# Kernel tuning notes

Hardware: AMD Instinct MI355X
Metric: run time of the kernel (lower is better)

The kernel has to match this reference:

```python
import jax, jax.numpy as jnp
import numpy as np
import math

HEAD_DIM = 256
NUM_HEADS = 8
NUM_KV_HEADS = 1
ROPE_THETA = 10000.0


def _rope_cos_sin(position_ids, dim, base, dtype):
    # inv_freq: [dim//2]
    inv_freq = 1.0 / (base ** (jnp.arange(0, dim, 2, dtype=jnp.float32) / dim))
    # freqs: [B, S, dim//2]
    freqs = position_ids.astype(jnp.float32)[..., None] * inv_freq[None, None, :]
    emb = jnp.concatenate([freqs, freqs], axis=-1)  # [B, S, dim]
    return jnp.cos(emb).astype(dtype), jnp.sin(emb).astype(dtype)


def _rotate_half(x):
    half = x.shape[-1] // 2
    return jnp.concatenate([-x[..., half:], x[..., :half]], axis=-1)


def setup_inputs() -> dict:
    key = jax.random.key(0)
    ks = jax.random.split(key, 6)
    B, S, H = 2, 2048, 2048
    hidden_states = jax.random.normal(ks[0], (B, S, H), dtype=jnp.float32)
    attention_mask = jnp.zeros((B, 1, S, S), dtype=jnp.float32)
    position_ids = jnp.arange(B * S, dtype=jnp.int64).reshape(B, S) % S
    wq = jax.random.normal(ks[1], (H, NUM_HEADS * HEAD_DIM), dtype=jnp.float32) * 0.02
    wk = jax.random.normal(ks[2], (H, NUM_KV_HEADS * HEAD_DIM), dtype=jnp.float32) * 0.02
    wv = jax.random.normal(ks[3], (H, NUM_KV_HEADS * HEAD_DIM), dtype=jnp.float32) * 0.02
    wo = jax.random.normal(ks[4], (NUM_HEADS * HEAD_DIM, H), dtype=jnp.float32) * 0.02
    return {"hidden_states": hidden_states, "attention_mask": attention_mask,
            "position_ids": position_ids, "wq": wq, "wk": wk, "wv": wv, "wo": wo}


def reference(hidden_states, attention_mask, position_ids, wq, wk, wv, wo):
    B, S, _ = hidden_states.shape
    q = (hidden_states @ wq).reshape(B, S, NUM_HEADS, HEAD_DIM).transpose(0, 2, 1, 3)
    k = (hidden_states @ wk).reshape(B, S, NUM_KV_HEADS, HEAD_DIM).transpose(0, 2, 1, 3)
    v = (hidden_states @ wv).reshape(B, S, NUM_KV_HEADS, HEAD_DIM).transpose(0, 2, 1, 3)

    cos, sin = _rope_cos_sin(position_ids, HEAD_DIM, ROPE_THETA, hidden_states.dtype)
    cos = cos[:, None, :, :]  # [B,1,S,D]
    sin = sin[:, None, :, :]
    q = q * cos + _rotate_half(q) * sin
    k = k * cos + _rotate_half(k) * sin

    # repeat_kv (GQA/MQA expansion)
    n_rep = NUM_HEADS // NUM_KV_HEADS
    k = jnp.repeat(k, n_rep, axis=1)  # [B,H,S,D]
    v = jnp.repeat(v, n_rep, axis=1)

    scores = jnp.einsum('bhqd,bhkd->bhqk', q, k) / math.sqrt(HEAD_DIM)
    scores = scores + attention_mask
    probs = jax.nn.softmax(scores.astype(jnp.float32), axis=-1).astype(q.dtype)
    attn = jnp.einsum('bhqk,bhkd->bhqd', probs, v)  # [B,H,S,D]
    attn = attn.transpose(0, 2, 1, 3).reshape(B, S, NUM_HEADS * HEAD_DIM)
    return attn @ wo
```

## Files before the change

### kernel.cpp

```cpp
#include <hip/hip_runtime.h>
#include <hip/hip_bf16.h>

typedef unsigned short u16;
using f32x4  = __attribute__((ext_vector_type(4))) float;
using bf16x8 = __attribute__((ext_vector_type(8))) __bf16;
using u16x8  = __attribute__((ext_vector_type(8))) unsigned short;
using u16x4  = __attribute__((ext_vector_type(4))) unsigned short;

__device__ __forceinline__ float bf2f(u16 v) {
  union { unsigned u; float f; } x; x.u = ((unsigned)v) << 16; return x.f;
}
__device__ __forceinline__ u16 f2bf(float f) {
  union { float f; unsigned u; } x; x.f = f;
  unsigned r = x.u + 0x7fffu + ((x.u >> 16) & 1u);
  return (u16)(r >> 16);
}
__device__ __forceinline__ void async_load16(const u16* g, u16* l) {
  __builtin_amdgcn_global_load_lds(
      (const __attribute__((address_space(1))) unsigned int*)g,
      (__attribute__((address_space(3))) unsigned int*)l, 16, 0, 0);
}
__device__ __forceinline__ float fexp2(float x) {
#if __has_builtin(__builtin_amdgcn_exp2f)
  return __builtin_amdgcn_exp2f(x);
#else
  return exp2f(x);
#endif
}
__device__ __forceinline__ float vmax4(f32x4 v) {
  return fmaxf(fmaxf(v[0], v[1]), fmaxf(v[2], v[3]));
}
__device__ __forceinline__ int swz_col(int col, int rowk) {
  return (col & ~63) | ((((col >> 3) & 7) ^ rowk) << 3) | (col & 7);
}

__global__ __launch_bounds__(256) void cast_f32_bf16_sw(const float* __restrict__ in,
                                                        u16* __restrict__ out) {
  long i = ((long)blockIdx.x * 256 + threadIdx.x) * 8;
  int m = (int)(i >> 11);
  int col = (int)(i & 2047);
  float4 a = *(const float4*)(in + i);
  float4 b = *(const float4*)(in + i + 4);
  u16x8 v;
  v[0] = f2bf(a.x); v[1] = f2bf(a.y); v[2] = f2bf(a.z); v[3] = f2bf(a.w);
  v[4] = f2bf(b.x); v[5] = f2bf(b.y); v[6] = f2bf(b.z); v[7] = f2bf(b.w);
  *(u16x8*)(out + ((long)m << 11) + swz_col(col, m & 7)) = v;
}

__global__ __launch_bounds__(256) void trans_all(const float* __restrict__ wq,
                                                 const float* __restrict__ wk,
                                                 const float* __restrict__ wv,
                                                 const float* __restrict__ wo,
                                                 u16* __restrict__ wqkvT, u16* __restrict__ woT) {
  const int z = blockIdx.z, bx = blockIdx.x, by = blockIdx.y;
  if (z == 1 && bx >= 64) return;
  const float* src; int srs; u16* dst;
  const int R0 = bx * 32;
  if (z == 0) {
    if (R0 < 2048)      { src = wq + R0;          srs = 2048; }
    else if (R0 < 2304) { src = wk + (R0 - 2048); srs = 256;  }
    else                { src = wv + (R0 - 2304); srs = 256;  }
    dst = wqkvT;
  } else { src = wo + R0; srs = 2048; dst = woT; }
  __shared__ float t[32][33];
  int tx = threadIdx.x, ty = threadIdx.y;
  int br = by * 32;
#pragma unroll
  for (int i = 0; i < 32; i += 8)
    t[ty + i][tx] = src[(long)(br + ty + i) * srs + tx];
  __syncthreads();
#pragma unroll
  for (int i = 0; i < 32; i += 8) {
    int R = R0 + ty + i, C = br + tx;
    dst[(long)R * 2048 + swz_col(C, R & 7)] = f2bf(t[tx][ty + i]);
  }
}

template <typename CT>
__global__ __launch_bounds__(256) void gemm_bt(const u16* __restrict__ A, const u16* __restrict__ Bt,
                                               CT* __restrict__ C, int M, int N, int K) {
  __shared__ __attribute__((aligned(16))) u16 sA[128 * 64];
  __shared__ __attribute__((aligned(16))) u16 sB[128 * 64];
  const int n0 = blockIdx.x * 128, m0 = blockIdx.y * 128;
  const int tid = threadIdx.x;
  const int w = tid >> 6, lane = tid & 63;
  const int l15 = lane & 15, quad = lane >> 4;
  const int wm = (w >> 1) * 64, wn = (w & 1) * 64;
  const int lrow = lane >> 3, lcol = (lane & 7) * 8;
  const u16* Ag = A + (long)(m0 + lrow) * K + lcol;
  const u16* Bg = Bt + (long)(n0 + lrow) * K + lcol;
  const int g0 = ((quad ^ (l15 & 7)) << 3);
  f32x4 acc[4][4] = {};
  for (int k0 = 0; k0 < K; k0 += 64) {
#pragma unroll
    for (int i = 0; i < 4; ++i) {
      int rr = (w * 4 + i) * 8;
      async_load16(Ag + (long)rr * K + k0, &sA[rr * 64]);
      async_load16(Bg + (long)rr * K + k0, &sB[rr * 64]);
    }
    __syncthreads();
#pragma unroll
    for (int kk2 = 0; kk2 < 2; ++kk2) {
      const int go = kk2 ? (g0 ^ 32) : g0;
      bf16x8 af[4], bf[4];
#pragma unroll
      for (int t = 0; t < 4; ++t) {
        af[t] = *(const bf16x8*)&sA[(wm + t * 16 + l15) * 64 + go];
        bf[t] = *(const bf16x8*)&sB[(wn + t * 16 + l15) * 64 + go];
      }
#pragma unroll
      for (int mt = 0; mt < 4; ++mt)
#pragma unroll
        for (int nt = 0; nt < 4; ++nt)
          acc[mt][nt] = __builtin_amdgcn_mfma_f32_16x16x32_bf16(af[mt], bf[nt], acc[mt][nt], 0, 0, 0);
    }
    __syncthreads();
  }
#pragma unroll
  for (int mt = 0; mt < 4; ++mt)
#pragma unroll
    for (int nt = 0; nt < 4; ++nt)
#pragma unroll
      for (int r = 0; r < 4; ++r) {
        long idx = (long)(m0 + wm + mt * 16 + quad * 4 + r) * N + (n0 + wn + nt * 16 + l15);
        if constexpr (sizeof(CT) == 4) C[idx] = acc[mt][nt][r];
        else                           C[idx] = f2bf(acc[mt][nt][r]);
      }
}

__global__ __launch_bounds__(256) void rope_pack(u16* __restrict__ qkv, u16* __restrict__ kp) {
  const int row = blockIdx.x;
  const int tid = threadIdx.x;
  const int d = tid & 127;
  const int s = row & 2047;
  float ang = (float)s * fexp2(-(float)d * 0.10381025296523007f);
  float sn, cs;
  sincosf(ang, &sn, &cs);
  long base = (long)row * 2560;
#pragma unroll
  for (int j = 0; j < 4; ++j) {
    int h = (tid >> 7) + j * 2;
    long p = base + h * 256 + d;
    float x0 = bf2f(qkv[p]), x1 = bf2f(qkv[p + 128]);
    qkv[p]       = f2bf(x0 * cs - x1 * sn);
    qkv[p + 128] = f2bf(x1 * cs + x0 * sn);
  }
  if (tid < 128) {
    long p = base + 2048 + d;
    float x0 = bf2f(qkv[p]), x1 = bf2f(qkv[p + 128]);
    float y0 = x0 * cs - x1 * sn, y1 = x1 * cs + x0 * sn;
    int b = row >> 11, t = (row >> 6) & 31, r = row & 63;
    long sw = (r >> 1) & 7;
    long tb = (long)(b * 32 + t) * 8 * 2048;
#pragma unroll
    for (int u = 0; u < 2; ++u) {
      int D = d + u * 128;
      long off = tb + (long)(D >> 5) * 2048 + r * 32 + (D & 31);
      long off2 = (((off >> 3) ^ sw) << 3) | (off & 7);
      kp[off2] = f2bf(u ? y1 : y0);
    }
  }
}

__global__ __launch_bounds__(256) void pack_vt(const u16* __restrict__ qkv, u16* __restrict__ vp) {
  __shared__ u16 sm[32][40];
  int x = blockIdx.x, y = blockIdx.y, b = blockIdx.z;
  int tx = threadIdx.x, ty = threadIdx.y;
  long inrow = (long)b * 2048 + (y >> 1) * 64 + (y & 1) * 32;
#pragma unroll
  for (int i = 0; i < 32; i += 8)
    sm[ty + i][tx] = qkv[(inrow + ty + i) * 2560 + 2304 + x * 32 + tx];
  __syncthreads();
  long obase = ((long)(b * 32 + (y >> 1)) * 2 + (y & 1)) * 8192 + (long)x * 1024;
#pragma unroll
  for (int i = 0; i < 32; i += 8) {
    long el = obase + (ty + i) * 32 + tx;
    el ^= (long)((((ty + i) >> 1) & 7) << 3);
    vp[el] = sm[tx][ty + i];
  }
}

__global__ __launch_bounds__(512) void flash_attn(const u16* __restrict__ qkv,
                                                  const u16* __restrict__ kp,
                                                  const u16* __restrict__ vp,
                                                  u16* __restrict__ attn) {
  const int qt = blockIdx.x, h = blockIdx.y, b = blockIdx.z;
  const int tid = threadIdx.x, w = tid >> 6, lane = tid & 63;
  const int l15 = lane & 15, quad = lane >> 4;
  __shared__ __attribute__((aligned(16))) u16 sK[2][16384];
  __shared__ __attribute__((aligned(16))) u16 sV[2][16384];
  __shared__ __attribute__((aligned(16))) u16 sP[8][1152];
  const long rowb = (long)b * 2048;
  const int qrow0 = qt * 128 + w * 16;
  const int swz_rd = (l15 >> 1) * 64 + ((((l15 & 1) << 2) | quad) ^ (l15 >> 1)) * 8;

  bf16x8 aq[8];
  {
    const u16* qp = qkv + (rowb + qrow0 + l15) * 2560 + h * 256 + quad * 8;
#pragma unroll
    for (int kk = 0; kk < 8; ++kk) aq[kk] = *(const bf16x8*)(qp + kk * 32);
  }

  float m_i = -1e30f, l_i = 0.f;
  f32x4 accO[16] = {};
  const float SC = 0.09016844005556021f;

  u16* Pw = &sP[w][0];
  const u16* kpb = kp + (long)b * 32 * 16384;
  const u16* vpb = vp + (long)b * 32 * 16384;

#pragma unroll
  for (int j = 0; j < 4; ++j) {
    int base = (w * 4 + j) * 512;
    async_load16(kpb + base + lane * 8, &sK[0][base]);
    async_load16(vpb + base + lane * 8, &sV[0][base]);
  }
  __syncthreads();

  for (int it = 0; it < 32; ++it) {
    const int cur = it & 1;
    const int nx = (it < 31) ? it + 1 : 31;
    const u16* ktn = kpb + (long)nx * 16384;
    const u16* vtn = vpb + (long)nx * 16384;
#pragma unroll
    for (int j = 0; j < 4; ++j) {
      int base = (w * 4 + j) * 512;
      async_load16(ktn + base + lane * 8, &sK[cur ^ 1][base]);
      async_load16(vtn + base + lane * 8, &sV[cur ^ 1][base]);
    }
    f32x4 sc[4] = {};
#pragma unroll
    for (int kk = 0; kk < 8; ++kk)
#pragma unroll
      for (int nt = 0; nt < 4; ++nt) {
        bf16x8 bk = *(const bf16x8*)&sK[cur][kk * 2048 + nt * 512 + swz_rd];
        sc[nt] = __builtin_amdgcn_mfma_f32_16x16x32_bf16(bk, aq[kk], sc[nt], 0, 0, 0);
      }
    float mx = fmaxf(fmaxf(vmax4(sc[0]), vmax4(sc[1])), fmaxf(vmax4(sc[2]), vmax4(sc[3]))) * SC;
    mx = fmaxf(mx, __shfl_xor(mx, 16, 64));
    mx = fmaxf(mx, __shfl_xor(mx, 32, 64));
    float mnew = fmaxf(m_i, mx);
    float al = fexp2(m_i - mnew);
    m_i = mnew;
    float rs = 0.f;
#pragma unroll
    for (int nt = 0; nt < 4; ++nt) {
      u16x4 pk;
#pragma unroll
      for (int r = 0; r < 4; ++r) {
        float pv = fexp2(sc[nt][r] * SC - mnew);
        rs += pv;
        pk[r] = f2bf(pv);
      }
      *(u16x4*)&Pw[l15 * 72 + nt * 16 + quad * 4] = pk;
    }
    rs += __shfl_xor(rs, 16, 64);
    rs += __shfl_xor(rs, 32, 64);
    l_i = l_i * al + rs;
    if (__any(al < 1.f)) {
#pragma unroll
      for (int r = 0; r < 4; ++r) {
        float ar = __shfl(al, quad * 4 + r, 16);
#pragma unroll
        for (int t = 0; t < 16; ++t) accO[t][r] *= ar;
      }
    }
    asm volatile("s_waitcnt lgkmcnt(0)" ::: "memory");
    bf16x8 pa0 = *(const bf16x8*)&Pw[l15 * 72 + quad * 8];
    bf16x8 pa1 = *(const bf16x8*)&Pw[l15 * 72 + 32 + quad * 8];
#pragma unroll
    for (int t = 0; t < 16; ++t) {
      bf16x8 bv0 = *(const bf16x8*)&sV[cur][t * 512 + swz_rd];
      bf16x8 bv1 = *(const bf16x8*)&sV[cur][8192 + t * 512 + swz_rd];
      accO[t] = __builtin_amdgcn_mfma_f32_16x16x32_bf16(pa0, bv0, accO[t], 0, 0, 0);
      accO[t] = __builtin_amdgcn_mfma_f32_16x16x32_bf16(pa1, bv1, accO[t], 0, 0, 0);
    }
    __syncthreads();
  }
  const int rw7 = 0;
#pragma unroll
  for (int r = 0; r < 4; ++r) {
    float lr = __shfl(l_i, quad * 4 + r, 16);
    float rinv = 1.f / lr;
    int key = (quad * 4 + r) & 7;
#pragma unroll
    for (int t = 0; t < 16; ++t) {
      int col = h * 256 + t * 16 + l15;
      attn[(rowb + qrow0 + quad * 4 + r) * 2048 + swz_col(col, key)] =
          f2bf(accO[t][r] * rinv);
    }
  }
  (void)rw7;
}

extern "C" void kernel_launch(void* const* d_in, const int* in_sizes, int n_in,
                              void* d_out, int out_size, void* d_ws, size_t ws_size,
                              hipStream_t stream) {
  const float* hidden = (const float*)d_in[0];
  const float* wq = (const float*)d_in[3];
  const float* wk = (const float*)d_in[4];
  const float* wv = (const float*)d_in[5];
  const float* wo = (const float*)d_in[6];
  float* out = (float*)d_out;

  char* ws = (char*)d_ws;
  u16* QKV   = (u16*)(ws);
  u16* WqkvT = (u16*)(ws + 20971520);
  u16* Kp    = (u16*)(ws + 20971520);
  u16* Vp    = (u16*)(ws + 23068672);
  u16* WoT   = (u16*)(ws + 31457280);
  u16* HB    = (u16*)(ws + 39845888);
  u16* ATT   = (u16*)(ws + 39845888);

  cast_f32_bf16_sw<<<4096, 256, 0, stream>>>(hidden, HB);
  trans_all<<<dim3(80, 64, 2), dim3(32, 8), 0, stream>>>(wq, wk, wv, wo, WqkvT, WoT);

  gemm_bt<u16><<<dim3(20, 32), dim3(256), 0, stream>>>(HB, WqkvT, QKV, 4096, 2560, 2048);

  rope_pack<<<4096, 256, 0, stream>>>(QKV, Kp);
  pack_vt<<<dim3(8, 64, 2), dim3(32, 8), 0, stream>>>(QKV, Vp);

  flash_attn<<<dim3(16, 8, 2), dim3(512), 0, stream>>>(QKV, Kp, Vp, ATT);

  gemm_bt<float><<<dim3(16, 32), dim3(256), 0, stream>>>(ATT, WoT, out, 4096, 2048, 2048);
}
```

Before: 340.5 us.

## Split attention tile into two halves with lazy max rescaling

Splits each 64-key attention tile into two 32-key halves so softmax of one half can interleave with the PV MFMAs of the other. Adds a lazy rescale that only updates the running max and rescales the accumulator when the new max exceeds the old by more than 8 (in log2 units), and defers the cross-lane row-sum reduction to the end. This cuts exp, shuffle and rescale work per iteration and exposes more MFMA/VALU overlap. The trade-offs are extra waitcnt points and probabilities that can reach up to 2^8 before normalization, which lowers bf16 headroom.

```diff
diff --git a/kernel.cpp b/kernel.cpp
--- a/kernel.cpp
+++ b/kernel.cpp
@@ -232,52 +232,104 @@
 #pragma unroll
     for (int kk = 0; kk < 8; ++kk)
 #pragma unroll
-      for (int nt = 0; nt < 4; ++nt) {
+      for (int nt = 0; nt < 2; ++nt) {
         bf16x8 bk = *(const bf16x8*)&sK[cur][kk * 2048 + nt * 512 + swz_rd];
         sc[nt] = __builtin_amdgcn_mfma_f32_16x16x32_bf16(bk, aq[kk], sc[nt], 0, 0, 0);
       }
-    float mx = fmaxf(fmaxf(vmax4(sc[0]), vmax4(sc[1])), fmaxf(vmax4(sc[2]), vmax4(sc[3]))) * SC;
-    mx = fmaxf(mx, __shfl_xor(mx, 16, 64));
-    mx = fmaxf(mx, __shfl_xor(mx, 32, 64));
-    float mnew = fmaxf(m_i, mx);
-    float al = fexp2(m_i - mnew);
-    m_i = mnew;
-    float rs = 0.f;
-#pragma unroll
-    for (int nt = 0; nt < 4; ++nt) {
-      u16x4 pk;
-#pragma unroll
-      for (int r = 0; r < 4; ++r) {
-        float pv = fexp2(sc[nt][r] * SC - mnew);
-        rs += pv;
-        pk[r] = f2bf(pv);
-      }
-      *(u16x4*)&Pw[l15 * 72 + nt * 16 + quad * 4] = pk;
-    }
-    rs += __shfl_xor(rs, 16, 64);
-    rs += __shfl_xor(rs, 32, 64);
-    l_i = l_i * al + rs;
-    if (__any(al < 1.f)) {
-#pragma unroll
-      for (int r = 0; r < 4; ++r) {
-        float ar = __shfl(al, quad * 4 + r, 16);
-#pragma unroll
-        for (int t = 0; t < 16; ++t) accO[t][r] *= ar;
-      }
+#pragma unroll
+    for (int kk = 0; kk < 8; ++kk)
+#pragma unroll
+      for (int nt = 2; nt < 4; ++nt) {
+        bf16x8 bk = *(const bf16x8*)&sK[cur][kk * 2048 + nt * 512 + swz_rd];
+        sc[nt] = __builtin_amdgcn_mfma_f32_16x16x32_bf16(bk, aq[kk], sc[nt], 0, 0, 0);
+      }
+
+    {
+      float mx = fmaxf(vmax4(sc[0]), vmax4(sc[1])) * SC;
+      float s1 = __shfl_xor(mx, 16, 64);
+      float s2 = __shfl_xor(mx, 32, 64);
+      float s3 = __shfl_xor(mx, 48, 64);
+      mx = fmaxf(fmaxf(mx, s1), fmaxf(s2, s3));
+      if (!__all(mx - m_i <= 8.f)) {
+        float mnew = fmaxf(m_i, mx);
+        float al = fexp2(m_i - mnew);
+        m_i = mnew;
+        l_i *= al;
+#pragma unroll
+        for (int r = 0; r < 4; ++r) {
+          float ar = __shfl(al, quad * 4 + r, 16);
+#pragma unroll
+          for (int t = 0; t < 16; ++t) accO[t][r] *= ar;
+        }
+      }
+      float rs = 0.f;
+#pragma unroll
+      for (int nt = 0; nt < 2; ++nt) {
+        u16x4 pk;
+#pragma unroll
+        for (int r = 0; r < 4; ++r) {
+          float pv = fexp2(sc[nt][r] * SC - m_i);
+          rs += pv;
+          pk[r] = f2bf(pv);
+        }
+        *(u16x4*)&Pw[l15 * 72 + nt * 16 + quad * 4] = pk;
+      }
+      l_i += rs;
     }
     asm volatile("s_waitcnt lgkmcnt(0)" ::: "memory");
     bf16x8 pa0 = *(const bf16x8*)&Pw[l15 * 72 + quad * 8];
-    bf16x8 pa1 = *(const bf16x8*)&Pw[l15 * 72 + 32 + quad * 8];
 #pragma unroll
     for (int t = 0; t < 16; ++t) {
       bf16x8 bv0 = *(const bf16x8*)&sV[cur][t * 512 + swz_rd];
+      accO[t] = __builtin_amdgcn_mfma_f32_16x16x32_bf16(pa0, bv0, accO[t], 0, 0, 0);
+    }
+    {
+      float mx = fmaxf(vmax4(sc[2]), vmax4(sc[3])) * SC;
+      float s1 = __shfl_xor(mx, 16, 64);
+      float s2 = __shfl_xor(mx, 32, 64);
+      float s3 = __shfl_xor(mx, 48, 64);
+      mx = fmaxf(fmaxf(mx, s1), fmaxf(s2, s3));
+      if (!__all(mx - m_i <= 8.f)) {
+        float mnew = fmaxf(m_i, mx);
+        float al = fexp2(m_i - mnew);
+        m_i = mnew;
+        l_i *= al;
+#pragma unroll
+        for (int r = 0; r < 4; ++r) {
+          float ar = __shfl(al, quad * 4 + r, 16);
+#pragma unroll
+          for (int t = 0; t < 16; ++t) accO[t][r] *= ar;
+        }
+      }
+      float rs = 0.f;
+#pragma unroll
+      for (int nt = 2; nt < 4; ++nt) {
+        u16x4 pk;
+#pragma unroll
+        for (int r = 0; r < 4; ++r) {
+          float pv = fexp2(sc[nt][r] * SC - m_i);
+          rs += pv;
+          pk[r] = f2bf(pv);
+        }
+        *(u16x4*)&Pw[l15 * 72 + nt * 16 + quad * 4] = pk;
+      }
+      l_i += rs;
+    }
+    asm volatile("s_waitcnt lgkmcnt(0)" ::: "memory");
+    bf16x8 pa1 = *(const bf16x8*)&Pw[l15 * 72 + 32 + quad * 8];
+#pragma unroll
+    for (int t = 0; t < 16; ++t) {
       bf16x8 bv1 = *(const bf16x8*)&sV[cur][8192 + t * 512 + swz_rd];
-      accO[t] = __builtin_amdgcn_mfma_f32_16x16x32_bf16(pa0, bv0, accO[t], 0, 0, 0);
       accO[t] = __builtin_amdgcn_mfma_f32_16x16x32_bf16(pa1, bv1, accO[t], 0, 0, 0);
     }
     __syncthreads();
   }
-  const int rw7 = 0;
+  {
+    float t1 = __shfl_xor(l_i, 16, 64);
+    float t2 = __shfl_xor(l_i, 32, 64);
+    float t3 = __shfl_xor(l_i, 48, 64);
+    l_i = (l_i + t1) + (t2 + t3);
+  }
 #pragma unroll
   for (int r = 0; r < 4; ++r) {
     float lr = __shfl(l_i, quad * 4 + r, 16);
@@ -290,7 +342,6 @@
           f2bf(accO[t][r] * rinv);
     }
   }
-  (void)rw7;
 }
 
 extern "C" void kernel_launch(void* const* d_in, const int* in_sizes, int n_in,
```

New measurement: 338.8 us. About the same (-0.5%).
